# Optimization experiments

Hardware: AMD Instinct MI355X
Metric: run time of the kernel (lower is better)

The kernel has to match this reference:

```python
import jax, jax.numpy as jnp
import numpy as np

T, S, A, H = 262144, 128, 8, 64
GAMMA, LAM, EPS_CLIP = 0.98, 0.95, 0.1


def setup_inputs() -> dict:
    key = jax.random.key(0)
    ks = jax.random.split(key, 14)
    s = jax.random.normal(ks[0], (T, S), jnp.float32)
    s_prime = jax.random.normal(ks[1], (T, S), jnp.float32)
    r = jax.random.normal(ks[2], (T, 1), jnp.float32)
    done_mask = jnp.ones((T, 1), jnp.float32)
    prob_a = jax.random.uniform(ks[3], (T, 1), jnp.float32) * 0.8 + 0.1
    a = jax.random.randint(ks[4], (T, 1), 0, A, dtype=jnp.int32)
    W1 = jax.random.normal(ks[5], (S, H), jnp.float32) / np.sqrt(S)
    b1 = jnp.zeros((H,), jnp.float32)
    W2 = jax.random.normal(ks[6], (H, H), jnp.float32) / np.sqrt(H)
    b2 = jnp.zeros((H,), jnp.float32)
    Wa = jax.random.normal(ks[7], (H, A), jnp.float32) / np.sqrt(H)
    ba = jnp.zeros((A,), jnp.float32)
    Wc = jax.random.normal(ks[8], (H, 1), jnp.float32) / np.sqrt(H)
    bc = jnp.zeros((1,), jnp.float32)
    return dict(s=s, s_prime=s_prime, r=r, done_mask=done_mask, prob_a=prob_a,
                a=a, W1=W1, b1=b1, W2=W2, b2=b2, Wa=Wa, ba=ba, Wc=Wc, bc=bc)


def _hidden(x, W1, b1, W2, b2):
    h = jax.nn.swish(x @ W1 + b1)
    return jax.nn.swish(h @ W2 + b2)


def reference(s, s_prime, r, done_mask, prob_a, a, W1, b1, W2, b2, Wa, ba, Wc, bc):
    h = _hidden(s, W1, b1, W2, b2)            # [T, H]
    v_s = h @ Wc + bc                         # [T, 1]
    hp = _hidden(s_prime, W1, b1, W2, b2)
    v_sp = hp @ Wc + bc                       # [T, 1]

    td_target = r + GAMMA * v_sp * done_mask  # [T, 1]
    delta = r + GAMMA * v_sp - v_s            # [T, 1] (no done mask, as in source)

    # Faithful replication of the source: transpose to (1, T) and reverse-scan
    # over the (size-1) leading axis, so advantage == delta (stop-gradient).
    delta_t = delta.T                         # [1, T]
    wd_t = jnp.full_like(delta_t, GAMMA * LAM)

    def step(acc, xs):
        wd, td = xs                           # each [T]
        new = td + wd * acc                   # [1, T]
        return new, new

    _, adv = jax.lax.scan(step, jnp.zeros_like(delta_t), (wd_t, delta_t), reverse=True)
    advantage = jax.lax.stop_gradient(adv.reshape(-1, 1))  # [T, 1]

    logits = h @ Wa + ba                      # [T, A]
    pi = jax.nn.softmax(logits, axis=-1)
    pi_a = jnp.take_along_axis(pi, a, axis=1) # [T, 1]

    ratio = jnp.exp(jnp.log(pi_a) - jnp.log(prob_a))
    surr1 = ratio * advantage
    surr2 = jnp.clip(ratio, 1.0 - EPS_CLIP, 1.0 + EPS_CLIP) * advantage

    err = jax.lax.stop_gradient(td_target) - v_s
    abs_err = jnp.abs(err)
    huber = jnp.mean(jnp.where(abs_err <= 1.0, 0.5 * err * err, abs_err - 0.5))

    return -jnp.minimum(surr1, surr2) + huber  # [T, 1]
```

## Files before the change

kernel.cpp:

```cpp
#include <hip/hip_runtime.h>
#include <cstddef>
#include <cstdint>

typedef __attribute__((ext_vector_type(8))) _Float16 f16x8;
typedef __attribute__((ext_vector_type(4))) float f32x4;

constexpr int S = 128;
constexpr int H = 64;
constexpr int A = 8;
constexpr float GAMMA = 0.98f;
constexpr float EPS_CLIP = 0.1f;

__device__ __forceinline__ float swishf(float x) {
    return x * __builtin_amdgcn_rcpf(1.0f + __expf(-x));
}
__device__ __forceinline__ f32x4 mfmaf(f16x8 a, f16x8 b, f32x4 c) {
    return __builtin_amdgcn_mfma_f32_16x16x32_f16(a, b, c, 0, 0, 0);
}

__global__ __launch_bounds__(256, 4) void ppo_fwd(
    const float* __restrict__ s, const float* __restrict__ sp,
    const int* __restrict__ aidx,
    const float* __restrict__ W1, const float* __restrict__ b1,
    const float* __restrict__ W2, const float* __restrict__ b2,
    const float* __restrict__ Wa, const float* __restrict__ ba,
    const float* __restrict__ Wc, const float* __restrict__ bc,
    float* __restrict__ ws_vs, float* __restrict__ ws_pia,
    float* __restrict__ ws_vsp, int nb)
{
    __shared__ f16x8 sW1[16][64];
    __shared__ f16x8 sW2[8][64];
    __shared__ f16x8 sWh[2][64];
    __shared__ __align__(16) _Float16 hbuf[4][16 * 72];
    __shared__ float hs[4][16 * 11];

    const int tid = threadIdx.x;
    const int pass = (blockIdx.x >= (unsigned)nb) ? 1 : 0;
    const int rb = blockIdx.x - pass * nb;
    const float* __restrict__ x = pass ? sp : s;

    for (int idx = tid; idx < 16 * 64; idx += 256) {
        int f = idx >> 6, ll = idx & 63;
        int nt = f >> 2, kk = f & 3;
        int gg = ll >> 4, col = nt * 16 + (ll & 15);
        f16x8 v;
        #pragma unroll
        for (int j = 0; j < 8; ++j)
            v[j] = (_Float16)W1[(kk * 32 + gg * 8 + j) * H + col];
        sW1[f][ll] = v;
    }
    for (int idx = tid; idx < 8 * 64; idx += 256) {
        int f = idx >> 6, ll = idx & 63;
        int nt = f >> 1, kk = f & 1;
        int gg = ll >> 4, col = nt * 16 + (ll & 15);
        f16x8 v;
        #pragma unroll
        for (int j = 0; j < 8; ++j)
            v[j] = (_Float16)W2[(kk * 32 + gg * 8 + j) * H + col];
        sW2[f][ll] = v;
    }
    for (int idx = tid; idx < 2 * 64; idx += 256) {
        int kk = idx >> 6, ll = idx & 63;
        int gg = ll >> 4, q = ll & 15;
        f16x8 v;
        #pragma unroll
        for (int j = 0; j < 8; ++j) {
            int k = kk * 32 + gg * 8 + j;
            v[j] = (_Float16)((q == 0) ? Wc[k] : ((q <= 8) ? Wa[k * A + (q - 1)] : 0.0f));
        }
        sWh[kk][ll] = v;
    }
    __syncthreads();

    const int w = tid >> 6, l = tid & 63, g = l >> 4, n15 = l & 15;
    _Float16* hb = hbuf[w];
    float* hsw = hs[w];

    float b1r[4], b2r[4];
    #pragma unroll
    for (int nt = 0; nt < 4; ++nt) { b1r[nt] = b1[nt * 16 + n15]; b2r[nt] = b2[nt * 16 + n15]; }
    const float bhr = (n15 == 0) ? bc[0] : ((n15 <= 8) ? ba[n15 - 1] : 0.0f);

    for (int mt2 = 0; mt2 < 2; ++mt2) {
        const int t0 = rb * 256 + w * 64 + mt2 * 32;

        f16x8 ax[2][4];
        #pragma unroll
        for (int tile = 0; tile < 2; ++tile) {
            const float* row = x + (size_t)(t0 + tile * 16 + n15) * S + g * 8;
            #pragma unroll
            for (int kk = 0; kk < 4; ++kk) {
                float4 v0 = *reinterpret_cast<const float4*>(row + kk * 32);
                float4 v1 = *reinterpret_cast<const float4*>(row + kk * 32 + 4);
                f16x8 a;
                a[0] = (_Float16)v0.x; a[1] = (_Float16)v0.y;
                a[2] = (_Float16)v0.z; a[3] = (_Float16)v0.w;
                a[4] = (_Float16)v1.x; a[5] = (_Float16)v1.y;
                a[6] = (_Float16)v1.z; a[7] = (_Float16)v1.w;
                ax[tile][kk] = a;
            }
        }
        int act[2] = {0, 0};
        if (pass == 0 && l < 16) {
            act[0] = aidx[t0 + l];
            act[1] = aidx[t0 + 16 + l];
        }

        f32x4 acc[2][4];
        #pragma unroll
        for (int tile = 0; tile < 2; ++tile)
            #pragma unroll
            for (int nt = 0; nt < 4; ++nt)
                acc[tile][nt] = (f32x4){b1r[nt], b1r[nt], b1r[nt], b1r[nt]};
        #pragma unroll
        for (int nt = 0; nt < 4; ++nt)
            #pragma unroll
            for (int kk = 0; kk < 4; ++kk) {
                f16x8 bw = sW1[nt * 4 + kk][l];
                acc[0][nt] = mfmaf(ax[0][kk], bw, acc[0][nt]);
                acc[1][nt] = mfmaf(ax[1][kk], bw, acc[1][nt]);
            }

        f16x8 a2[2][2];
        #pragma unroll
        for (int tile = 0; tile < 2; ++tile) {
            #pragma unroll
            for (int nt = 0; nt < 4; ++nt)
                #pragma unroll
                for (int rj = 0; rj < 4; ++rj)
                    hb[(g * 4 + rj) * 72 + nt * 16 + n15] =
                        (_Float16)swishf(acc[tile][nt][rj]);
            #pragma unroll
            for (int kk = 0; kk < 2; ++kk)
                a2[tile][kk] = *reinterpret_cast<f16x8*>(&hb[n15 * 72 + kk * 32 + g * 8]);
        }

        f32x4 acc2[2][4];
        #pragma unroll
        for (int tile = 0; tile < 2; ++tile)
            #pragma unroll
            for (int nt = 0; nt < 4; ++nt)
                acc2[tile][nt] = (f32x4){b2r[nt], b2r[nt], b2r[nt], b2r[nt]};
        #pragma unroll
        for (int nt = 0; nt < 4; ++nt)
            #pragma unroll
            for (int kk = 0; kk < 2; ++kk) {
                f16x8 bw = sW2[nt * 2 + kk][l];
                acc2[0][nt] = mfmaf(a2[0][kk], bw, acc2[0][nt]);
                acc2[1][nt] = mfmaf(a2[1][kk], bw, acc2[1][nt]);
            }

        f16x8 a3[2][2];
        #pragma unroll
        for (int tile = 0; tile < 2; ++tile) {
            #pragma unroll
            for (int nt = 0; nt < 4; ++nt)
                #pragma unroll
                for (int rj = 0; rj < 4; ++rj)
                    hb[(g * 4 + rj) * 72 + nt * 16 + n15] =
                        (_Float16)swishf(acc2[tile][nt][rj]);
            #pragma unroll
            for (int kk = 0; kk < 2; ++kk)
                a3[tile][kk] = *reinterpret_cast<f16x8*>(&hb[n15 * 72 + kk * 32 + g * 8]);
        }

        f32x4 ah[2] = {(f32x4){bhr, bhr, bhr, bhr}, (f32x4){bhr, bhr, bhr, bhr}};
        #pragma unroll
        for (int kk = 0; kk < 2; ++kk) {
            f16x8 bw = sWh[kk][l];
            ah[0] = mfmaf(a3[0][kk], bw, ah[0]);
            ah[1] = mfmaf(a3[1][kk], bw, ah[1]);
        }

        if (pass == 1) {
            #pragma unroll
            for (int tile = 0; tile < 2; ++tile)
                if (n15 == 0) {
                    #pragma unroll
                    for (int rj = 0; rj < 4; ++rj)
                        ws_vsp[t0 + tile * 16 + g * 4 + rj] = ah[tile][rj];
                }
        } else {
            #pragma unroll
            for (int tile = 0; tile < 2; ++tile) {
                if (n15 <= 8) {
                    #pragma unroll
                    for (int rj = 0; rj < 4; ++rj)
                        hsw[(g * 4 + rj) * 11 + n15] = ah[tile][rj];
                }
                if (l < 16) {
                    float vs = hsw[l * 11 + 0];
                    float lgq[A];
                    float m = -1e30f;
                    #pragma unroll
                    for (int q = 0; q < A; ++q) {
                        lgq[q] = hsw[l * 11 + 1 + q];
                        m = fmaxf(m, lgq[q]);
                    }
                    float den = 0.f, num = 0.f;
                    #pragma unroll
                    for (int q = 0; q < A; ++q) {
                        float e = __expf(lgq[q] - m);
                        den += e;
                        num = (q == act[tile]) ? e : num;
                    }
                    int t = t0 + tile * 16 + l;
                    ws_vs[t]  = vs;
                    ws_pia[t] = num / den;
                }
            }
        }
    }
}

__global__ __launch_bounds__(256) void ppo_epi(
    const float* __restrict__ r, const float* __restrict__ done,
    const float* __restrict__ prob_a,
    const float* __restrict__ ws_vs, const float* __restrict__ ws_pia,
    const float* __restrict__ ws_vsp,
    float* __restrict__ out, float* __restrict__ partial, int Ttot)
{
    __shared__ float sred[256];
    const int tid = threadIdx.x;
    const int t = blockIdx.x * 256 + tid;

    float he = 0.f;
    if (t < Ttot) {
        float vs  = ws_vs[t];
        float vsp = ws_vsp[t];
        float rr  = r[t];
        float dm  = done[t];
        float ratio = ws_pia[t] / prob_a[t];

        float td_target = fmaf(GAMMA * dm, vsp, rr);
        float delta     = rr + GAMMA * vsp - vs;
        float s1 = ratio * delta;
        float rcl = fminf(fmaxf(ratio, 1.0f - EPS_CLIP), 1.0f + EPS_CLIP);
        float s2 = rcl * delta;
        out[t] = -fminf(s1, s2);

        float err = td_target - vs;
        float ae = fabsf(err);
        he = (ae <= 1.0f) ? (0.5f * err * err) : (ae - 0.5f);
    }

    sred[tid] = he;
    __syncthreads();
    #pragma unroll
    for (int off = 128; off > 0; off >>= 1) {
        if (tid < off) sred[tid] += sred[tid + off];
        __syncthreads();
    }
    if (tid == 0) partial[blockIdx.x] = sred[0];
}

__global__ __launch_bounds__(256) void ppo_reduce(float* __restrict__ partial,
                                                  int nblocks, float invT)
{
    __shared__ float sred[256];
    float v = 0.f;
    for (int i = threadIdx.x; i < nblocks; i += 256) v += partial[i];
    sred[threadIdx.x] = v;
    __syncthreads();
    #pragma unroll
    for (int off = 128; off > 0; off >>= 1) {
        if (threadIdx.x < off) sred[threadIdx.x] += sred[threadIdx.x + off];
        __syncthreads();
    }
    if (threadIdx.x == 0) partial[nblocks] = sred[0] * invT;
}

__global__ __launch_bounds__(256) void ppo_add(float4* __restrict__ out4,
                                               const float* __restrict__ meanp, int n4)
{
    int i = blockIdx.x * blockDim.x + threadIdx.x;
    if (i < n4) {
        float m = meanp[0];
        float4 v = out4[i];
        v.x += m; v.y += m; v.z += m; v.w += m;
        out4[i] = v;
    }
}

extern "C" void kernel_launch(void* const* d_in, const int* in_sizes, int n_in,
                              void* d_out, int out_size, void* d_ws, size_t ws_size,
                              hipStream_t stream)
{
    const float* s      = (const float*)d_in[0];
    const float* sp     = (const float*)d_in[1];
    const float* r      = (const float*)d_in[2];
    const float* done   = (const float*)d_in[3];
    const float* prob_a = (const float*)d_in[4];
    const int*   a      = (const int*)d_in[5];
    const float* W1     = (const float*)d_in[6];
    const float* b1     = (const float*)d_in[7];
    const float* W2     = (const float*)d_in[8];
    const float* b2     = (const float*)d_in[9];
    const float* Wa     = (const float*)d_in[10];
    const float* ba     = (const float*)d_in[11];
    const float* Wc     = (const float*)d_in[12];
    const float* bc     = (const float*)d_in[13];

    float* out = (float*)d_out;
    float* ws  = (float*)d_ws;

    const int Ttot = in_sizes[0] / S;
    const int nb   = Ttot / 256;

    float* ws_vs  = ws;
    float* ws_pia = ws + Ttot;
    float* ws_vsp = ws + 2 * (size_t)Ttot;
    float* partial = ws + 3 * (size_t)Ttot;

    ppo_fwd<<<2 * nb, 256, 0, stream>>>(s, sp, a, W1, b1, W2, b2, Wa, ba, Wc, bc,
                                        ws_vs, ws_pia, ws_vsp, nb);
    ppo_epi<<<nb, 256, 0, stream>>>(r, done, prob_a, ws_vs, ws_pia, ws_vsp,
                                    out, partial, Ttot);
    ppo_reduce<<<1, 256, 0, stream>>>(partial, nb, 1.0f / (float)Ttot);

    const int n4 = Ttot / 4;
    ppo_add<<<(n4 + 255) / 256, 256, 0, stream>>>((float4*)out, partial + nb, n4);
}
```

Before: 65.15 us.

## Fuse s and s' passes with epilogue into one kernel and merge reduce/add

Each block now processes both s and s_prime for the same 128 rows. Value, policy and loss terms are computed in-register, so the workspace round-trip for v_s, pi_a and v_sp goes away, along with the separate epilogue kernel. Loads for the second 16-row chunk are software-prefetched while the first chunk computes. The final mean reduction and the broadcast add are merged into one kernel where every block re-reduces the partials. Costs are higher register pressure (occupancy hint lowered to 3) and a redundant reduction in each finishing block.

```diff
diff --git a/kernel.cpp b/kernel.cpp
--- a/kernel.cpp
+++ b/kernel.cpp
@@ -18,26 +18,45 @@
     return __builtin_amdgcn_mfma_f32_16x16x32_f16(a, b, c, 0, 0, 0);
 }
 
-__global__ __launch_bounds__(256, 4) void ppo_fwd(
+__global__ __launch_bounds__(256, 3) void ppo_fused(
     const float* __restrict__ s, const float* __restrict__ sp,
-    const int* __restrict__ aidx,
+    const float* __restrict__ r, const float* __restrict__ done,
+    const float* __restrict__ prob_a, const int* __restrict__ aidx,
     const float* __restrict__ W1, const float* __restrict__ b1,
     const float* __restrict__ W2, const float* __restrict__ b2,
     const float* __restrict__ Wa, const float* __restrict__ ba,
     const float* __restrict__ Wc, const float* __restrict__ bc,
-    float* __restrict__ ws_vs, float* __restrict__ ws_pia,
-    float* __restrict__ ws_vsp, int nb)
+    float* __restrict__ out, float* __restrict__ partial)
 {
     __shared__ f16x8 sW1[16][64];
     __shared__ f16x8 sW2[8][64];
     __shared__ f16x8 sWh[2][64];
     __shared__ __align__(16) _Float16 hbuf[4][16 * 72];
     __shared__ float hs[4][16 * 11];
+    __shared__ float sred[256];
 
     const int tid = threadIdx.x;
-    const int pass = (blockIdx.x >= (unsigned)nb) ? 1 : 0;
-    const int rb = blockIdx.x - pass * nb;
-    const float* __restrict__ x = pass ? sp : s;
+    const int w = tid >> 6, l = tid & 63, g = l >> 4, n15 = l & 15;
+    const int base = blockIdx.x * 128 + w * 32;
+
+    float4 raw[16];
+    {
+        const float* p0 = s  + (size_t)(base + n15) * S + g * 8;
+        const float* p1 = sp + (size_t)(base + n15) * S + g * 8;
+        #pragma unroll
+        for (int kk = 0; kk < 4; ++kk) {
+            raw[kk * 2]         = *reinterpret_cast<const float4*>(p0 + kk * 32);
+            raw[kk * 2 + 1]     = *reinterpret_cast<const float4*>(p0 + kk * 32 + 4);
+            raw[8 + kk * 2]     = *reinterpret_cast<const float4*>(p1 + kk * 32);
+            raw[8 + kk * 2 + 1] = *reinterpret_cast<const float4*>(p1 + kk * 32 + 4);
+        }
+    }
+    float rrv[2], dmv[2], pav[2];
+    int actv[2] = {0, 0};
+    if (l < 16) {
+        const int t = base + l;
+        rrv[0] = r[t]; dmv[0] = done[t]; pav[0] = prob_a[t]; actv[0] = aidx[t];
+    }
 
     for (int idx = tid; idx < 16 * 64; idx += 256) {
         int f = idx >> 6, ll = idx & 63;
@@ -72,26 +91,26 @@
     }
     __syncthreads();
 
-    const int w = tid >> 6, l = tid & 63, g = l >> 4, n15 = l & 15;
-    _Float16* hb = hbuf[w];
-    float* hsw = hs[w];
-
     float b1r[4], b2r[4];
     #pragma unroll
     for (int nt = 0; nt < 4; ++nt) { b1r[nt] = b1[nt * 16 + n15]; b2r[nt] = b2[nt * 16 + n15]; }
     const float bhr = (n15 == 0) ? bc[0] : ((n15 <= 8) ? ba[n15 - 1] : 0.0f);
 
-    for (int mt2 = 0; mt2 < 2; ++mt2) {
-        const int t0 = rb * 256 + w * 64 + mt2 * 32;
+    _Float16* hb = hbuf[w];
+    float* hsw = hs[w];
+    float hacc = 0.f;
+
+    #pragma unroll
+    for (int c = 0; c < 2; ++c) {
+        const int t0 = base + c * 16;
 
         f16x8 ax[2][4];
         #pragma unroll
-        for (int tile = 0; tile < 2; ++tile) {
-            const float* row = x + (size_t)(t0 + tile * 16 + n15) * S + g * 8;
+        for (int tile = 0; tile < 2; ++tile)
             #pragma unroll
             for (int kk = 0; kk < 4; ++kk) {
-                float4 v0 = *reinterpret_cast<const float4*>(row + kk * 32);
-                float4 v1 = *reinterpret_cast<const float4*>(row + kk * 32 + 4);
+                float4 v0 = raw[tile * 8 + kk * 2];
+                float4 v1 = raw[tile * 8 + kk * 2 + 1];
                 f16x8 a;
                 a[0] = (_Float16)v0.x; a[1] = (_Float16)v0.y;
                 a[2] = (_Float16)v0.z; a[3] = (_Float16)v0.w;
@@ -99,11 +118,21 @@
                 a[6] = (_Float16)v1.z; a[7] = (_Float16)v1.w;
                 ax[tile][kk] = a;
             }
-        }
-        int act[2] = {0, 0};
-        if (pass == 0 && l < 16) {
-            act[0] = aidx[t0 + l];
-            act[1] = aidx[t0 + 16 + l];
+
+        if (c == 0) {
+            const float* p0 = s  + (size_t)(base + 16 + n15) * S + g * 8;
+            const float* p1 = sp + (size_t)(base + 16 + n15) * S + g * 8;
+            #pragma unroll
+            for (int kk = 0; kk < 4; ++kk) {
+                raw[kk * 2]         = *reinterpret_cast<const float4*>(p0 + kk * 32);
+                raw[kk * 2 + 1]     = *reinterpret_cast<const float4*>(p0 + kk * 32 + 4);
+                raw[8 + kk * 2]     = *reinterpret_cast<const float4*>(p1 + kk * 32);
+                raw[8 + kk * 2 + 1] = *reinterpret_cast<const float4*>(p1 + kk * 32 + 4);
+            }
+            if (l < 16) {
+                const int t = base + 16 + l;
+                rrv[1] = r[t]; dmv[1] = done[t]; pav[1] = prob_a[t]; actv[1] = aidx[t];
+            }
         }
 
         f32x4 acc[2][4];
@@ -172,79 +201,46 @@
             ah[1] = mfmaf(a3[1][kk], bw, ah[1]);
         }
 
-        if (pass == 1) {
-            #pragma unroll
-            for (int tile = 0; tile < 2; ++tile)
-                if (n15 == 0) {
-                    #pragma unroll
-                    for (int rj = 0; rj < 4; ++rj)
-                        ws_vsp[t0 + tile * 16 + g * 4 + rj] = ah[tile][rj];
-                }
-        } else {
-            #pragma unroll
-            for (int tile = 0; tile < 2; ++tile) {
-                if (n15 <= 8) {
-                    #pragma unroll
-                    for (int rj = 0; rj < 4; ++rj)
-                        hsw[(g * 4 + rj) * 11 + n15] = ah[tile][rj];
-                }
-                if (l < 16) {
-                    float vs = hsw[l * 11 + 0];
-                    float lgq[A];
-                    float m = -1e30f;
-                    #pragma unroll
-                    for (int q = 0; q < A; ++q) {
-                        lgq[q] = hsw[l * 11 + 1 + q];
-                        m = fmaxf(m, lgq[q]);
-                    }
-                    float den = 0.f, num = 0.f;
-                    #pragma unroll
-                    for (int q = 0; q < A; ++q) {
-                        float e = __expf(lgq[q] - m);
-                        den += e;
-                        num = (q == act[tile]) ? e : num;
-                    }
-                    int t = t0 + tile * 16 + l;
-                    ws_vs[t]  = vs;
-                    ws_pia[t] = num / den;
-                }
-            }
-        }
-    }
-}
-
-__global__ __launch_bounds__(256) void ppo_epi(
-    const float* __restrict__ r, const float* __restrict__ done,
-    const float* __restrict__ prob_a,
-    const float* __restrict__ ws_vs, const float* __restrict__ ws_pia,
-    const float* __restrict__ ws_vsp,
-    float* __restrict__ out, float* __restrict__ partial, int Ttot)
-{
-    __shared__ float sred[256];
-    const int tid = threadIdx.x;
-    const int t = blockIdx.x * 256 + tid;
-
-    float he = 0.f;
-    if (t < Ttot) {
-        float vs  = ws_vs[t];
-        float vsp = ws_vsp[t];
-        float rr  = r[t];
-        float dm  = done[t];
-        float ratio = ws_pia[t] / prob_a[t];
-
-        float td_target = fmaf(GAMMA * dm, vsp, rr);
-        float delta     = rr + GAMMA * vsp - vs;
-        float s1 = ratio * delta;
-        float rcl = fminf(fmaxf(ratio, 1.0f - EPS_CLIP), 1.0f + EPS_CLIP);
-        float s2 = rcl * delta;
-        out[t] = -fminf(s1, s2);
-
-        float err = td_target - vs;
-        float ae = fabsf(err);
-        he = (ae <= 1.0f) ? (0.5f * err * err) : (ae - 0.5f);
-    }
-
-    sred[tid] = he;
+        #pragma unroll
+        for (int rj = 0; rj < 4; ++rj) {
+            if (n15 <= 8) hsw[(g * 4 + rj) * 11 + n15] = ah[0][rj];
+            if (n15 == 0) hsw[(g * 4 + rj) * 11 + 9]  = ah[1][rj];
+        }
+
+        if (l < 16) {
+            float vs = hsw[l * 11 + 0];
+            float lgq[A];
+            float m = -1e30f;
+            #pragma unroll
+            for (int q = 0; q < A; ++q) {
+                lgq[q] = hsw[l * 11 + 1 + q];
+                m = fmaxf(m, lgq[q]);
+            }
+            float den = 0.f, num = 0.f;
+            #pragma unroll
+            for (int q = 0; q < A; ++q) {
+                float e = __expf(lgq[q] - m);
+                den += e;
+                num = (q == actv[c]) ? e : num;
+            }
+            float pia = num / den;
+            float vsp = hsw[l * 11 + 9];
+
+            float ratio = pia / pav[c];
+            float td    = fmaf(GAMMA * dmv[c], vsp, rrv[c]);
+            float dlt   = rrv[c] + GAMMA * vsp - vs;
+            float s1 = ratio * dlt;
+            float rcl = fminf(fmaxf(ratio, 1.0f - EPS_CLIP), 1.0f + EPS_CLIP);
+            float s2 = rcl * dlt;
+            out[t0 + l] = -fminf(s1, s2);
+
+            float err = td - vs;
+            float ae = fabsf(err);
+            hacc += (ae <= 1.0f) ? (0.5f * err * err) : (ae - 0.5f);
+        }
+    }
+
+    sred[tid] = hacc;
     __syncthreads();
     #pragma unroll
     for (int off = 128; off > 0; off >>= 1) {
@@ -254,31 +250,27 @@
     if (tid == 0) partial[blockIdx.x] = sred[0];
 }
 
-__global__ __launch_bounds__(256) void ppo_reduce(float* __restrict__ partial,
-                                                  int nblocks, float invT)
+__global__ __launch_bounds__(256) void ppo_finish(
+    const float* __restrict__ partial, int nparts, float invT,
+    float4* __restrict__ out4, int n4)
 {
     __shared__ float sred[256];
+    const int tid = threadIdx.x;
     float v = 0.f;
-    for (int i = threadIdx.x; i < nblocks; i += 256) v += partial[i];
-    sred[threadIdx.x] = v;
+    for (int i = tid; i < nparts; i += 256) v += partial[i];
+    sred[tid] = v;
     __syncthreads();
     #pragma unroll
     for (int off = 128; off > 0; off >>= 1) {
-        if (threadIdx.x < off) sred[threadIdx.x] += sred[threadIdx.x + off];
+        if (tid < off) sred[tid] += sred[tid + off];
         __syncthreads();
     }
-    if (threadIdx.x == 0) partial[nblocks] = sred[0] * invT;
-}
-
-__global__ __launch_bounds__(256) void ppo_add(float4* __restrict__ out4,
-                                               const float* __restrict__ meanp, int n4)
-{
-    int i = blockIdx.x * blockDim.x + threadIdx.x;
+    const float m = sred[0] * invT;
+    const int i = blockIdx.x * 256 + tid;
     if (i < n4) {
-        float m = meanp[0];
-        float4 v = out4[i];
-        v.x += m; v.y += m; v.z += m; v.w += m;
-        out4[i] = v;
+        float4 o = out4[i];
+        o.x += m; o.y += m; o.z += m; o.w += m;
+        out4[i] = o;
     }
 }
 
@@ -302,22 +294,17 @@
     const float* bc     = (const float*)d_in[13];
 
     float* out = (float*)d_out;
-    float* ws  = (float*)d_ws;
+    float* partial = (float*)d_ws;
 
     const int Ttot = in_sizes[0] / S;
-    const int nb   = Ttot / 256;
-
-    float* ws_vs  = ws;
-    float* ws_pia = ws + Ttot;
-    float* ws_vsp = ws + 2 * (size_t)Ttot;
-    float* partial = ws + 3 * (size_t)Ttot;
-
-    ppo_fwd<<<2 * nb, 256, 0, stream>>>(s, sp, a, W1, b1, W2, b2, Wa, ba, Wc, bc,
-                                        ws_vs, ws_pia, ws_vsp, nb);
-    ppo_epi<<<nb, 256, 0, stream>>>(r, done, prob_a, ws_vs, ws_pia, ws_vsp,
-                                    out, partial, Ttot);
-    ppo_reduce<<<1, 256, 0, stream>>>(partial, nb, 1.0f / (float)Ttot);
+    const int nb2  = Ttot / 128;
+
+    ppo_fused<<<nb2, 256, 0, stream>>>(s, sp, r, done, prob_a, a,
+                                       W1, b1, W2, b2, Wa, ba, Wc, bc,
+                                       out, partial);
 
     const int n4 = Ttot / 4;
-    ppo_add<<<(n4 + 255) / 256, 256, 0, stream>>>((float4*)out, partial + nb, n4);
-}
+    ppo_finish<<<(n4 + 255) / 256, 256, 0, stream>>>(partial, nb2,
+                                                     1.0f / (float)Ttot,
+                                                     (float4*)out, n4);
+}
```

Result: slower. 87.78 us (+34.7%).

## Prefetch input rows before weight staging and merge reduce with add kernel

Applied to the files above, without the earlier changes.

The forward kernel now issues the global loads for the first 32 input rows before staging the weights into shared memory, and prefetches the second 32 rows while the first half is being computed. This hides global-load latency behind weight setup and MFMA work. The occupancy hint drops from 4 to 3 blocks per SM to make room for the extra registers. Separately, the single-block reduce and the add kernel become one kernel in which every block redundantly sums the 1024 partials, saving one launch at the cost of repeated tiny reductions.

```diff
diff --git a/kernel.cpp b/kernel.cpp
--- a/kernel.cpp
+++ b/kernel.cpp
@@ -18,7 +18,7 @@
     return __builtin_amdgcn_mfma_f32_16x16x32_f16(a, b, c, 0, 0, 0);
 }
 
-__global__ __launch_bounds__(256, 4) void ppo_fwd(
+__global__ __launch_bounds__(256, 3) void ppo_fwd(
     const float* __restrict__ s, const float* __restrict__ sp,
     const int* __restrict__ aidx,
     const float* __restrict__ W1, const float* __restrict__ b1,
@@ -39,6 +39,35 @@
     const int rb = blockIdx.x - pass * nb;
     const float* __restrict__ x = pass ? sp : s;
 
+    const int w = tid >> 6, l = tid & 63, g = l >> 4, n15 = l & 15;
+    const int wbase = rb * 256 + w * 64;
+
+    float4 raw[16];
+    {
+        const float* p0 = x + (size_t)(wbase + n15) * S + g * 8;
+        const float* p1 = x + (size_t)(wbase + 16 + n15) * S + g * 8;
+        #pragma unroll
+        for (int kk = 0; kk < 4; ++kk) {
+            raw[kk * 2]         = *reinterpret_cast<const float4*>(p0 + kk * 32);
+            raw[kk * 2 + 1]     = *reinterpret_cast<const float4*>(p0 + kk * 32 + 4);
+            raw[8 + kk * 2]     = *reinterpret_cast<const float4*>(p1 + kk * 32);
+            raw[8 + kk * 2 + 1] = *reinterpret_cast<const float4*>(p1 + kk * 32 + 4);
+        }
+    }
+    float b1r[4], b2r[4];
+    #pragma unroll
+    for (int nt = 0; nt < 4; ++nt) { b1r[nt] = b1[nt * 16 + n15]; b2r[nt] = b2[nt * 16 + n15]; }
+    const float bhr = (n15 == 0) ? bc[0] : ((n15 <= 8) ? ba[n15 - 1] : 0.0f);
+    int act[2][2] = {{0, 0}, {0, 0}};
+    if (pass == 0 && l < 16) {
+        #pragma unroll
+        for (int mt2 = 0; mt2 < 2; ++mt2) {
+            act[mt2][0] = aidx[wbase + mt2 * 32 + l];
+            act[mt2][1] = aidx[wbase + mt2 * 32 + 16 + l];
+        }
+    }
+    asm volatile("" ::: "memory");
+
     for (int idx = tid; idx < 16 * 64; idx += 256) {
         int f = idx >> 6, ll = idx & 63;
         int nt = f >> 2, kk = f & 3;
@@ -72,26 +101,20 @@
     }
     __syncthreads();
 
-    const int w = tid >> 6, l = tid & 63, g = l >> 4, n15 = l & 15;
     _Float16* hb = hbuf[w];
     float* hsw = hs[w];
 
-    float b1r[4], b2r[4];
     #pragma unroll
-    for (int nt = 0; nt < 4; ++nt) { b1r[nt] = b1[nt * 16 + n15]; b2r[nt] = b2[nt * 16 + n15]; }
-    const float bhr = (n15 == 0) ? bc[0] : ((n15 <= 8) ? ba[n15 - 1] : 0.0f);
-
     for (int mt2 = 0; mt2 < 2; ++mt2) {
-        const int t0 = rb * 256 + w * 64 + mt2 * 32;
+        const int t0 = wbase + mt2 * 32;
 
         f16x8 ax[2][4];
         #pragma unroll
-        for (int tile = 0; tile < 2; ++tile) {
-            const float* row = x + (size_t)(t0 + tile * 16 + n15) * S + g * 8;
+        for (int tile = 0; tile < 2; ++tile)
             #pragma unroll
             for (int kk = 0; kk < 4; ++kk) {
-                float4 v0 = *reinterpret_cast<const float4*>(row + kk * 32);
-                float4 v1 = *reinterpret_cast<const float4*>(row + kk * 32 + 4);
+                float4 v0 = raw[tile * 8 + kk * 2];
+                float4 v1 = raw[tile * 8 + kk * 2 + 1];
                 f16x8 a;
                 a[0] = (_Float16)v0.x; a[1] = (_Float16)v0.y;
                 a[2] = (_Float16)v0.z; a[3] = (_Float16)v0.w;
@@ -99,11 +122,18 @@
                 a[6] = (_Float16)v1.z; a[7] = (_Float16)v1.w;
                 ax[tile][kk] = a;
             }
-        }
-        int act[2] = {0, 0};
-        if (pass == 0 && l < 16) {
-            act[0] = aidx[t0 + l];
-            act[1] = aidx[t0 + 16 + l];
+
+        if (mt2 == 0) {
+            const float* p0 = x + (size_t)(wbase + 32 + n15) * S + g * 8;
+            const float* p1 = x + (size_t)(wbase + 48 + n15) * S + g * 8;
+            #pragma unroll
+            for (int kk = 0; kk < 4; ++kk) {
+                raw[kk * 2]         = *reinterpret_cast<const float4*>(p0 + kk * 32);
+                raw[kk * 2 + 1]     = *reinterpret_cast<const float4*>(p0 + kk * 32 + 4);
+                raw[8 + kk * 2]     = *reinterpret_cast<const float4*>(p1 + kk * 32);
+                raw[8 + kk * 2 + 1] = *reinterpret_cast<const float4*>(p1 + kk * 32 + 4);
+            }
+            asm volatile("" ::: "memory");
         }
 
         f32x4 acc[2][4];
@@ -202,7 +232,7 @@
                     for (int q = 0; q < A; ++q) {
                         float e = __expf(lgq[q] - m);
                         den += e;
-                        num = (q == act[tile]) ? e : num;
+                        num = (q == act[mt2][tile]) ? e : num;
                     }
                     int t = t0 + tile * 16 + l;
                     ws_vs[t]  = vs;
@@ -254,31 +284,27 @@
     if (tid == 0) partial[blockIdx.x] = sred[0];
 }
 
-__global__ __launch_bounds__(256) void ppo_reduce(float* __restrict__ partial,
-                                                  int nblocks, float invT)
+__global__ __launch_bounds__(256) void ppo_finish(
+    const float* __restrict__ partial, int nparts, float invT,
+    float4* __restrict__ out4, int n4)
 {
     __shared__ float sred[256];
+    const int tid = threadIdx.x;
     float v = 0.f;
-    for (int i = threadIdx.x; i < nblocks; i += 256) v += partial[i];
-    sred[threadIdx.x] = v;
+    for (int i = tid; i < nparts; i += 256) v += partial[i];
+    sred[tid] = v;
     __syncthreads();
     #pragma unroll
     for (int off = 128; off > 0; off >>= 1) {
-        if (threadIdx.x < off) sred[threadIdx.x] += sred[threadIdx.x + off];
+        if (tid < off) sred[tid] += sred[tid + off];
         __syncthreads();
     }
-    if (threadIdx.x == 0) partial[nblocks] = sred[0] * invT;
-}
-
-__global__ __launch_bounds__(256) void ppo_add(float4* __restrict__ out4,
-                                               const float* __restrict__ meanp, int n4)
-{
-    int i = blockIdx.x * blockDim.x + threadIdx.x;
+    const float m = sred[0] * invT;
+    const int i = blockIdx.x * 256 + tid;
     if (i < n4) {
-        float m = meanp[0];
-        float4 v = out4[i];
-        v.x += m; v.y += m; v.z += m; v.w += m;
-        out4[i] = v;
+        float4 o = out4[i];
+        o.x += m; o.y += m; o.z += m; o.w += m;
+        out4[i] = o;
     }
 }
 
@@ -316,8 +342,9 @@
                                         ws_vs, ws_pia, ws_vsp, nb);
     ppo_epi<<<nb, 256, 0, stream>>>(r, done, prob_a, ws_vs, ws_pia, ws_vsp,
                                     out, partial, Ttot);
-    ppo_reduce<<<1, 256, 0, stream>>>(partial, nb, 1.0f / (float)Ttot);
 
     const int n4 = Ttot / 4;
-    ppo_add<<<(n4 + 255) / 256, 256, 0, stream>>>((float4*)out, partial + nb, n4);
-}
+    ppo_finish<<<(n4 + 255) / 256, 256, 0, stream>>>(partial, nb,
+                                                     1.0f / (float)Ttot,
+                                                     (float4*)out, n4);
+}
```

Result: slower. 75.11 us (+15.3%).
